# Optimization experiments

Measured on AMD Instinct MI355X. Metric: run time of the kernel, lower is better.

The kernel has to match this reference:

```python
import jax
import jax.numpy as jnp
from jax import lax
import numpy as np

E = 4          # num_experts
CIN = 128
COUT = 128
K = 3
STAT = 6
HID = 16       # router hidden width
STRIDE = 1
PAD = 1


def setup_inputs() -> dict:
    key = jax.random.key(0)
    ks = jax.random.split(key, 8)
    B, H, W = 32, 64, 64
    x = jax.random.normal(ks[0], (B, CIN, H, W), dtype=jnp.float32)
    scene_stats = jax.random.normal(ks[1], (B, STAT), dtype=jnp.float32)
    # router: Linear(stat_dim,16) -> ReLU -> Linear(16,E) -> Softmax
    W1 = jax.random.normal(ks[2], (HID, STAT), dtype=jnp.float32) * (1.0 / np.sqrt(STAT))
    b1 = jnp.zeros((HID,), dtype=jnp.float32)
    W2 = jax.random.normal(ks[3], (E, HID), dtype=jnp.float32) * (1.0 / np.sqrt(HID))
    b2 = jnp.zeros((E,), dtype=jnp.float32)
    weight_experts = jax.random.normal(ks[4], (E, COUT, CIN, K, K), dtype=jnp.float32) * 0.02
    bias_experts = jnp.zeros((E, COUT), dtype=jnp.float32)
    return {"x": x, "scene_stats": scene_stats, "W1": W1, "b1": b1,
            "W2": W2, "b2": b2, "weight_experts": weight_experts,
            "bias_experts": bias_experts}


def reference(x, scene_stats, W1, b1, W2, b2, weight_experts, bias_experts):
    B, Cin, H, W = x.shape
    Cout = weight_experts.shape[1]
    # router
    h = jax.nn.relu(scene_stats @ W1.T + b1)                 # [B, HID]
    routing = jax.nn.softmax(h @ W2.T + b2, axis=1)          # [B, E]
    # per-sample dynamic weights / bias
    dyn_w = jnp.einsum('bk,koihw->boihw', routing, weight_experts)  # [B,Cout,Cin,K,K]
    dyn_b = jnp.einsum('bk,ko->bo', routing, bias_experts)          # [B,Cout]
    # grouped conv with groups = B (each sample uses its own filter bank)
    x_r = x.reshape(1, B * Cin, H, W)
    w_r = dyn_w.reshape(B * Cout, Cin, K, K)
    out = lax.conv_general_dilated(
        x_r, w_r,
        window_strides=(STRIDE, STRIDE),
        padding=((PAD, PAD), (PAD, PAD)),
        feature_group_count=B,
        dimension_numbers=('NCHW', 'OIHW', 'NCHW'))
    out = out.reshape(B, Cout, out.shape[2], out.shape[3])
    return out + dyn_b[:, :, None, None]
```

## Files before the change

kernel.cpp:

```cpp
#include <hip/hip_runtime.h>
#include <hip/hip_bf16.h>


typedef short bf16x8 __attribute__((ext_vector_type(8)));
typedef float f32x4  __attribute__((ext_vector_type(4)));

#define VMWAIT(n) asm volatile("s_waitcnt vmcnt(" #n ")" ::: "memory")

static __device__ __forceinline__ unsigned short f2bf(float f) {
    unsigned u = __float_as_uint(f);
    u = u + 0x7FFFu + ((u >> 16) & 1u);
    return (unsigned short)(u >> 16);
}

static __device__ __forceinline__ void gl2lds16(const unsigned short* g, unsigned short* l) {
    __builtin_amdgcn_global_load_lds(
        (const __attribute__((address_space(1))) unsigned int*)g,
        (__attribute__((address_space(3))) unsigned int*)l,
        16, 0, 0);
}

__global__ void prep_kernel(const float* __restrict__ stats, const float* __restrict__ W1,
                            const float* __restrict__ b1, const float* __restrict__ W2,
                            const float* __restrict__ b2, const float* __restrict__ wexp,
                            const float* __restrict__ bexp, unsigned short* __restrict__ dynw,
                            float* __restrict__ dynb)
{
    __shared__ float ls[4*1152];
    __shared__ float lr[32*4];
    const int tid = threadIdx.x;
    const int co  = blockIdx.x & 127;
    const int bg  = blockIdx.x >> 7;

    if (tid < 32) {
        float s[6];
#pragma unroll
        for (int i = 0; i < 6; ++i) s[i] = stats[tid*6 + i];
        float h[16];
#pragma unroll
        for (int j = 0; j < 16; ++j) {
            float a = b1[j];
#pragma unroll
            for (int i = 0; i < 6; ++i) a += W1[j*6+i]*s[i];
            h[j] = a > 0.f ? a : 0.f;
        }
        float lg[4];
#pragma unroll
        for (int e = 0; e < 4; ++e) {
            float a = b2[e];
#pragma unroll
            for (int j = 0; j < 16; ++j) a += W2[e*16+j]*h[j];
            lg[e] = a;
        }
        float m = fmaxf(fmaxf(lg[0],lg[1]), fmaxf(lg[2],lg[3]));
        float ex[4], sum = 0.f;
#pragma unroll
        for (int e = 0; e < 4; ++e) { ex[e] = expf(lg[e]-m); sum += ex[e]; }
        float inv = 1.f / sum;
#pragma unroll
        for (int e = 0; e < 4; ++e) lr[tid*4+e] = ex[e]*inv;
    }
    for (int i = tid; i < 4*1152; i += 256) {
        int e = i / 1152, j = i - e*1152;
        ls[i] = wexp[((unsigned long long)(e*128 + co))*1152 + j];
    }
    __syncthreads();

    if (bg == 0 && tid < 32) {
        float sb = 0.f;
#pragma unroll
        for (int e = 0; e < 4; ++e) sb += lr[tid*4+e] * bexp[e*128 + co];
        dynb[tid*128 + co] = sb;
    }

    const int ci  = tid & 127;
    const int tp0 = tid >> 7;
    const int cic = ci >> 5;
    const int g   = (ci >> 3) & 3;
    const int jj  = ci & 7;
    const int mi  = co >> 4;
    const int l15 = co & 15;
    for (int bb = bg*8; bb < bg*8 + 8; ++bb) {
        float r0 = lr[bb*4+0], r1 = lr[bb*4+1], r2 = lr[bb*4+2], r3 = lr[bb*4+3];
#pragma unroll
        for (int pp = 0; pp < 5; ++pp) {
            int tap = 2*pp + tp0;
            if (tap < 9) {
                int j = ci*9 + tap;
                float v = r0*ls[j] + r1*ls[1152+j] + r2*ls[2*1152+j] + r3*ls[3*1152+j];
                dynw[((((unsigned long long)(bb*4 + cic)*9 + tap)*8 + mi)*64 + g*16 + l15)*8 + jj] = f2bf(v);
            }
        }
    }
}

__global__ __launch_bounds__(256, 2) void conv_kernel(
    const float* __restrict__ x,
    const unsigned short* __restrict__ dynw,
    const float* __restrict__ dynb,
    float* __restrict__ out)
{
    __shared__ __align__(16) unsigned short xs[6*66*32];
    __shared__ __align__(16) unsigned short wsm[6][4096];

    const int tid  = threadIdx.x;
    const int wave = tid >> 6;
    const int lane = tid & 63;
    const int l15  = lane & 15;
    const int g    = lane >> 4;
    const int so    = tid & 7;
    const int scg   = (tid >> 3) & 3;
    const int scolO = (tid >> 5) & 7;

    int bidx = ((blockIdx.x & 7) << 6) | (blockIdx.x >> 3);
    const int b  = bidx >> 4;
    const int r0 = (bidx & 15) << 2;

    f32x4 acc[8][4];
#pragma unroll
    for (int mi = 0; mi < 8; ++mi)
#pragma unroll
        for (int ni = 0; ni < 4; ++ni) acc[mi][ni] = (f32x4){0.f,0.f,0.f,0.f};

    const float* xsrcb = x + (unsigned long long)b*(128ull*64*64);
    const unsigned short* wsrcb = dynw + (unsigned long long)b*(4ull*9*4096);

#define XISSUE(kk)                                                             \
    do {                                                                       \
        int grow_ = r0 + (kk) - 1;                                             \
        int growc_ = grow_ < 0 ? 0 : (grow_ > 63 ? 63 : grow_);                \
        const float* xp_ = xsrcb + (((unsigned long long)(cic_*32 + scg*8 + so))*64 \
                            + growc_)*64 + scolO*8;                            \
        xv[(kk)%3][0] = *(const float4*)xp_;                                   \
        xv[(kk)%3][1] = *(const float4*)(xp_ + 4);                             \
    } while (0)

#define XPROC(kk)                                                              \
    do {                                                                       \
        int grow_ = r0 + (kk) - 1;                                             \
        bool oob_ = (grow_ < 0) || (grow_ > 63);                               \
        float4 v0 = xv[(kk)%3][0], v1 = xv[(kk)%3][1];                         \
        unsigned ra = oob_ ? 0u : (f2bf(v0.x) | ((unsigned)f2bf(v0.y) << 16)); \
        unsigned rb = oob_ ? 0u : (f2bf(v0.z) | ((unsigned)f2bf(v0.w) << 16)); \
        unsigned rc = oob_ ? 0u : (f2bf(v1.x) | ((unsigned)f2bf(v1.y) << 16)); \
        unsigned rd = oob_ ? 0u : (f2bf(v1.z) | ((unsigned)f2bf(v1.w) << 16)); \
        unsigned pa = __shfl_xor(ra,1), pb = __shfl_xor(rb,1);                 \
        unsigned pc = __shfl_xor(rc,1), pd = __shfl_xor(rd,1);                 \
        bool oddl = so & 1;                                                    \
        unsigned sa = oddl ? ((pa>>16)|(ra&0xFFFF0000u)) : ((ra&0xFFFFu)|(pa<<16)); \
        unsigned sb = oddl ? ((pb>>16)|(rb&0xFFFF0000u)) : ((rb&0xFFFFu)|(pb<<16)); \
        unsigned sc = oddl ? ((pc>>16)|(rc&0xFFFF0000u)) : ((rc&0xFFFFu)|(pc<<16)); \
        unsigned sd = oddl ? ((pd>>16)|(rd&0xFFFF0000u)) : ((rd&0xFFFFu)|(pd<<16)); \
        unsigned qa = __shfl_xor(sa,2), qb = __shfl_xor(sb,2);                 \
        unsigned qc = __shfl_xor(sc,2), qd = __shfl_xor(sd,2);                 \
        bool hi2 = so & 2;                                                     \
        unsigned A0 = hi2 ? qc : sa, A1 = hi2 ? sc : qa;                       \
        unsigned B0 = hi2 ? qd : sb, B1 = hi2 ? sd : qb;                       \
        int cA_ = (so & 1) + (hi2 ? 4 : 0);                                    \
        int half8_ = (so >> 2) << 3;                                           \
        int lcolA_ = scolO*8 + cA_ + 1;                                        \
        int lcolB_ = lcolA_ + 2;                                               \
        int byteA_ = ((kk)*66 + lcolA_)*64 + (((scg + (lcolA_>>1)) & 3)<<4) + half8_; \
        int byteB_ = ((kk)*66 + lcolB_)*64 + (((scg + (lcolB_>>1)) & 3)<<4) + half8_; \
        *(uint2*)((char*)xs + byteA_) = make_uint2(A0, A1);                    \
        *(uint2*)((char*)xs + byteB_) = make_uint2(B0, B1);                    \
    } while (0)

#define XSTAGE(CIC_, WFIRST_, DRAIN_)                                          \
    do {                                                                       \
        const int cic_ = (CIC_);                                               \
        float4 xv[3][2];                                                       \
        XISSUE(0); XISSUE(1);                                                  \
        _Pragma("unroll")                                                      \
        for (int t = 0; t < 3; ++t) {                                          \
            const unsigned short* wsrc_ = wsrcb + (unsigned)(((WFIRST_) + t)*4096); \
            unsigned short* wd_ = wsm[((WFIRST_) + t) % 6];                    \
            gl2lds16(wsrc_ + (unsigned)tid*8,       wd_ + (unsigned)tid*8);    \
            gl2lds16(wsrc_ + (unsigned)(tid+256)*8, wd_ + (unsigned)(tid+256)*8); \
        }                                                                      \
        VMWAIT(8); XPROC(0); XISSUE(2);                                        \
        VMWAIT(8); XPROC(1); XISSUE(3);                                        \
        VMWAIT(8); XPROC(2); XISSUE(4);                                        \
        VMWAIT(8); XPROC(3); XISSUE(5);                                        \
        VMWAIT(8); XPROC(4);                                                   \
        if (DRAIN_) { VMWAIT(0); } else { VMWAIT(6); }                         \
        XPROC(5);                                                              \
    } while (0)

    if (tid < 48) {
        int zrow = tid >> 3, zcol = ((tid >> 2) & 1) ? 65 : 0, zch = tid & 3;
        *(uint4*)((char*)xs + (zrow*66 + zcol)*64 + zch*16) = make_uint4(0,0,0,0);
    }
    XSTAGE(0, 0, true);
    asm volatile("s_waitcnt lgkmcnt(0)" ::: "memory");
    __syncthreads();

#pragma unroll
    for (int p = 0; p < 12; ++p) {
        const int cic = p / 3;
        if (p > 0) {
            VMWAIT(0);
            __builtin_amdgcn_s_barrier();
            __builtin_amdgcn_sched_barrier(0);
        }
        if ((p % 3) == 0 && p > 0) {
            XSTAGE(cic, 3*p + 3, false);
            asm volatile("s_waitcnt lgkmcnt(0)" ::: "memory");
            __builtin_amdgcn_s_barrier();
            __builtin_amdgcn_sched_barrier(0);
        } else if (p < 11) {
#pragma unroll
            for (int t = 0; t < 3; ++t) {
                const int s = 3*p + 3 + t;
                const unsigned short* wsrc = wsrcb + (unsigned)(s*4096);
                unsigned short* wd = wsm[s % 6];
                gl2lds16(wsrc + (unsigned)tid*8,       wd + (unsigned)tid*8);
                gl2lds16(wsrc + (unsigned)(tid+256)*8, wd + (unsigned)(tid+256)*8);
            }
        }
        const int ky   = p % 3;
        const int lrow = wave + ky;
        __builtin_amdgcn_s_setprio(1);
#pragma unroll
        for (int kx = 0; kx < 3; ++kx) {
            const unsigned short* wb = wsm[(3*p + kx) % 6];
            bf16x8 afrag[8];
#pragma unroll
            for (int mi = 0; mi < 8; ++mi)
                afrag[mi] = *(const bf16x8*)(wb + (unsigned)((mi*64 + lane)*8));
#pragma unroll
            for (int ni = 0; ni < 4; ++ni) {
                int lcol = 16*ni + l15 + kx;
                int boff = (lrow*66 + lcol)*64 + (((g + (lcol >> 1)) & 3) << 4);
                bf16x8 bfrag = *(const bf16x8*)((const char*)xs + boff);
#pragma unroll
                for (int mi = 0; mi < 8; ++mi)
                    acc[mi][ni] = __builtin_amdgcn_mfma_f32_16x16x32_bf16(
                                      afrag[mi], bfrag, acc[mi][ni], 0, 0, 0);
            }
        }
        __builtin_amdgcn_s_setprio(0);
    }

    const int y = r0 + wave;
#pragma unroll
    for (int mi = 0; mi < 8; ++mi) {
#pragma unroll
        for (int r = 0; r < 4; ++r) {
            int co = 16*mi + g*4 + r;
            float bias = dynb[b*128 + co];
            float* op = out + (((unsigned long long)(b*128 + co))*64 + y)*64;
#pragma unroll
            for (int ni = 0; ni < 4; ++ni)
                op[16*ni + l15] = acc[mi][ni][r] + bias;
        }
    }
#undef XSTAGE
#undef XPROC
#undef XISSUE
}

extern "C" void kernel_launch(void* const* d_in, const int* in_sizes, int n_in,
                              void* d_out, int out_size, void* d_ws, size_t ws_size,
                              hipStream_t stream)
{
    const float* x     = (const float*)d_in[0];
    const float* stats = (const float*)d_in[1];
    const float* W1    = (const float*)d_in[2];
    const float* b1    = (const float*)d_in[3];
    const float* W2    = (const float*)d_in[4];
    const float* b2    = (const float*)d_in[5];
    const float* wexp  = (const float*)d_in[6];
    const float* bexp  = (const float*)d_in[7];
    float* out = (float*)d_out;

    char* ws = (char*)d_ws;
    float* dynb           = (float*)(ws + 512);
    unsigned short* dynw  = (unsigned short*)(ws + 32768);

    prep_kernel<<<512, 256, 0, stream>>>(stats, W1, b1, W2, b2, wexp, bexp, dynw, dynb);
    conv_kernel<<<512, 256, 0, stream>>>(x, dynw, dynb, out);
}
```

Baseline: 59.58 us.

## Stage input tile via two-phase LDS transpose instead of shuffle-based packing

The input staging now loads float4 strips from two channels per thread, packs channel pairs into bf16 words, and writes them to LDS in a row-major scratch layout. A second phase reads them back transposed and writes the swizzled channel-innermost layout the MFMA loop expects. This replaces the cross-lane shuffle network and the narrower global loads with wider coalesced row loads. The cost is two extra barriers and an LDS round trip per stage, and the VM wait overlap with the weight prefetch changes.

```diff
diff --git a/kernel.cpp b/kernel.cpp
--- a/kernel.cpp
+++ b/kernel.cpp
@@ -6,6 +6,7 @@
 typedef float f32x4  __attribute__((ext_vector_type(4)));
 
 #define VMWAIT(n) asm volatile("s_waitcnt vmcnt(" #n ")" ::: "memory")
+#define LGKM0()   asm volatile("s_waitcnt lgkmcnt(0)" ::: "memory")
 
 static __device__ __forceinline__ unsigned short f2bf(float f) {
     unsigned u = __float_as_uint(f);
@@ -108,9 +109,10 @@
     const int lane = tid & 63;
     const int l15  = lane & 15;
     const int g    = lane >> 4;
-    const int so    = tid & 7;
-    const int scg   = (tid >> 3) & 3;
-    const int scolO = (tid >> 5) & 7;
+    const int pr    = tid >> 4;
+    const int c4    = tid & 15;
+    const int p2col = tid & 63;
+    const int p2cg  = tid >> 6;
 
     int bidx = ((blockIdx.x & 7) << 6) | (blockIdx.x >> 3);
     const int b  = bidx >> 4;
@@ -125,52 +127,32 @@
     const float* xsrcb = x + (unsigned long long)b*(128ull*64*64);
     const unsigned short* wsrcb = dynw + (unsigned long long)b*(4ull*9*4096);
 
-#define XISSUE(kk)                                                             \
+#define P1ISSUE(kk)                                                            \
     do {                                                                       \
         int grow_ = r0 + (kk) - 1;                                             \
         int growc_ = grow_ < 0 ? 0 : (grow_ > 63 ? 63 : grow_);                \
-        const float* xp_ = xsrcb + (((unsigned long long)(cic_*32 + scg*8 + so))*64 \
-                            + growc_)*64 + scolO*8;                            \
+        const float* xp_ = xsrcb + (unsigned)((cic_*32 + 2*pr)*4096)           \
+                         + growc_*64 + c4*4;                                   \
         xv[(kk)%3][0] = *(const float4*)xp_;                                   \
-        xv[(kk)%3][1] = *(const float4*)(xp_ + 4);                             \
+        xv[(kk)%3][1] = *(const float4*)(xp_ + 4096);                          \
     } while (0)
 
-#define XPROC(kk)                                                              \
+#define P1PROC(kk)                                                             \
     do {                                                                       \
         int grow_ = r0 + (kk) - 1;                                             \
         bool oob_ = (grow_ < 0) || (grow_ > 63);                               \
-        float4 v0 = xv[(kk)%3][0], v1 = xv[(kk)%3][1];                         \
-        unsigned ra = oob_ ? 0u : (f2bf(v0.x) | ((unsigned)f2bf(v0.y) << 16)); \
-        unsigned rb = oob_ ? 0u : (f2bf(v0.z) | ((unsigned)f2bf(v0.w) << 16)); \
-        unsigned rc = oob_ ? 0u : (f2bf(v1.x) | ((unsigned)f2bf(v1.y) << 16)); \
-        unsigned rd = oob_ ? 0u : (f2bf(v1.z) | ((unsigned)f2bf(v1.w) << 16)); \
-        unsigned pa = __shfl_xor(ra,1), pb = __shfl_xor(rb,1);                 \
-        unsigned pc = __shfl_xor(rc,1), pd = __shfl_xor(rd,1);                 \
-        bool oddl = so & 1;                                                    \
-        unsigned sa = oddl ? ((pa>>16)|(ra&0xFFFF0000u)) : ((ra&0xFFFFu)|(pa<<16)); \
-        unsigned sb = oddl ? ((pb>>16)|(rb&0xFFFF0000u)) : ((rb&0xFFFFu)|(pb<<16)); \
-        unsigned sc = oddl ? ((pc>>16)|(rc&0xFFFF0000u)) : ((rc&0xFFFFu)|(pc<<16)); \
-        unsigned sd = oddl ? ((pd>>16)|(rd&0xFFFF0000u)) : ((rd&0xFFFFu)|(pd<<16)); \
-        unsigned qa = __shfl_xor(sa,2), qb = __shfl_xor(sb,2);                 \
-        unsigned qc = __shfl_xor(sc,2), qd = __shfl_xor(sd,2);                 \
-        bool hi2 = so & 2;                                                     \
-        unsigned A0 = hi2 ? qc : sa, A1 = hi2 ? sc : qa;                       \
-        unsigned B0 = hi2 ? qd : sb, B1 = hi2 ? sd : qb;                       \
-        int cA_ = (so & 1) + (hi2 ? 4 : 0);                                    \
-        int half8_ = (so >> 2) << 3;                                           \
-        int lcolA_ = scolO*8 + cA_ + 1;                                        \
-        int lcolB_ = lcolA_ + 2;                                               \
-        int byteA_ = ((kk)*66 + lcolA_)*64 + (((scg + (lcolA_>>1)) & 3)<<4) + half8_; \
-        int byteB_ = ((kk)*66 + lcolB_)*64 + (((scg + (lcolB_>>1)) & 3)<<4) + half8_; \
-        *(uint2*)((char*)xs + byteA_) = make_uint2(A0, A1);                    \
-        *(uint2*)((char*)xs + byteB_) = make_uint2(B0, B1);                    \
+        float4 va_ = xv[(kk)%3][0], vb_ = xv[(kk)%3][1];                       \
+        unsigned w0_ = oob_ ? 0u : (f2bf(va_.x) | ((unsigned)f2bf(vb_.x) << 16)); \
+        unsigned w1_ = oob_ ? 0u : (f2bf(va_.y) | ((unsigned)f2bf(vb_.y) << 16)); \
+        unsigned w2_ = oob_ ? 0u : (f2bf(va_.z) | ((unsigned)f2bf(vb_.z) << 16)); \
+        unsigned w3_ = oob_ ? 0u : (f2bf(va_.w) | ((unsigned)f2bf(vb_.w) << 16)); \
+        *(uint4*)((char*)xs + (kk)*4224 + pr*256 + c4*16)                      \
+            = make_uint4(w0_, w1_, w2_, w3_);                                  \
     } while (0)
 
-#define XSTAGE(CIC_, WFIRST_, DRAIN_)                                          \
+#define XSTAGE2(CIC_, WFIRST_)                                                 \
     do {                                                                       \
         const int cic_ = (CIC_);                                               \
-        float4 xv[3][2];                                                       \
-        XISSUE(0); XISSUE(1);                                                  \
         _Pragma("unroll")                                                      \
         for (int t = 0; t < 3; ++t) {                                          \
             const unsigned short* wsrc_ = wsrcb + (unsigned)(((WFIRST_) + t)*4096); \
@@ -178,22 +160,47 @@
             gl2lds16(wsrc_ + (unsigned)tid*8,       wd_ + (unsigned)tid*8);    \
             gl2lds16(wsrc_ + (unsigned)(tid+256)*8, wd_ + (unsigned)(tid+256)*8); \
         }                                                                      \
-        VMWAIT(8); XPROC(0); XISSUE(2);                                        \
-        VMWAIT(8); XPROC(1); XISSUE(3);                                        \
-        VMWAIT(8); XPROC(2); XISSUE(4);                                        \
-        VMWAIT(8); XPROC(3); XISSUE(5);                                        \
-        VMWAIT(8); XPROC(4);                                                   \
-        if (DRAIN_) { VMWAIT(0); } else { VMWAIT(6); }                         \
-        XPROC(5);                                                              \
+        float4 xv[3][2];                                                       \
+        P1ISSUE(0); P1ISSUE(1); P1ISSUE(2);                                    \
+        VMWAIT(4); P1PROC(0); P1ISSUE(3);                                      \
+        VMWAIT(4); P1PROC(1); P1ISSUE(4);                                      \
+        VMWAIT(4); P1PROC(2); P1ISSUE(5);                                      \
+        VMWAIT(4); P1PROC(3);                                                  \
+        VMWAIT(2); P1PROC(4);                                                  \
+        VMWAIT(0); P1PROC(5);                                                  \
+        LGKM0();                                                               \
+        __builtin_amdgcn_s_barrier();                                          \
+        __builtin_amdgcn_sched_barrier(0);                                     \
+        uint4 tv[6];                                                           \
+        _Pragma("unroll")                                                      \
+        for (int r = 0; r < 6; ++r) {                                          \
+            const char* rb_ = (const char*)xs + r*4224 + p2cg*1024 + p2col*4;  \
+            tv[r].x = *(const unsigned*)(rb_);                                 \
+            tv[r].y = *(const unsigned*)(rb_ + 256);                           \
+            tv[r].z = *(const unsigned*)(rb_ + 512);                           \
+            tv[r].w = *(const unsigned*)(rb_ + 768);                           \
+        }                                                                      \
+        LGKM0();                                                               \
+        __builtin_amdgcn_s_barrier();                                          \
+        __builtin_amdgcn_sched_barrier(0);                                     \
+        {                                                                      \
+            int lcol_ = p2col + 1;                                             \
+            int wb_   = ((p2cg + (lcol_ >> 1)) & 3) << 4;                      \
+            _Pragma("unroll")                                                  \
+            for (int r = 0; r < 6; ++r)                                        \
+                *(uint4*)((char*)xs + r*4224 + lcol_*64 + wb_) = tv[r];        \
+        }                                                                      \
+        if (tid < 24)                                                          \
+            *(uint4*)((char*)xs + (tid>>2)*4224 + (tid&3)*16)                  \
+                = make_uint4(0,0,0,0);                                         \
+        LGKM0();                                                               \
+        __builtin_amdgcn_s_barrier();                                          \
+        __builtin_amdgcn_sched_barrier(0);                                     \
     } while (0)
 
-    if (tid < 48) {
-        int zrow = tid >> 3, zcol = ((tid >> 2) & 1) ? 65 : 0, zch = tid & 3;
-        *(uint4*)((char*)xs + (zrow*66 + zcol)*64 + zch*16) = make_uint4(0,0,0,0);
-    }
-    XSTAGE(0, 0, true);
-    asm volatile("s_waitcnt lgkmcnt(0)" ::: "memory");
-    __syncthreads();
+    if (tid < 24)
+        *(uint4*)((char*)xs + (tid>>2)*4224 + 65*64 + (tid&3)*16) = make_uint4(0,0,0,0);
+    XSTAGE2(0, 0);
 
 #pragma unroll
     for (int p = 0; p < 12; ++p) {
@@ -204,10 +211,7 @@
             __builtin_amdgcn_sched_barrier(0);
         }
         if ((p % 3) == 0 && p > 0) {
-            XSTAGE(cic, 3*p + 3, false);
-            asm volatile("s_waitcnt lgkmcnt(0)" ::: "memory");
-            __builtin_amdgcn_s_barrier();
-            __builtin_amdgcn_sched_barrier(0);
+            XSTAGE2(cic, 3*p + 3);
         } else if (p < 11) {
 #pragma unroll
             for (int t = 0; t < 3; ++t) {
@@ -255,9 +259,9 @@
                 op[16*ni + l15] = acc[mi][ni][r] + bias;
         }
     }
-#undef XSTAGE
-#undef XPROC
-#undef XISSUE
+#undef XSTAGE2
+#undef P1PROC
+#undef P1ISSUE
 }
 
 extern "C" void kernel_launch(void* const* d_in, const int* in_sizes, int n_in,
```

New measurement: 65.08 us. 9.2% more time.
